# Kernel optimization log

Measured on AMD Instinct MI355X. Metric: run time of the kernel, lower is better.

The kernel has to match this reference:

```python
import jax, jax.numpy as jnp
import numpy as np

B, L, C = 2, 2048, 1024
H = 16
HD = C // H  # head_features = 64


def setup_inputs() -> dict:
    key = jax.random.key(0)
    k1, k2, k3, k4, k5, k6 = jax.random.split(key, 6)
    input_x = jax.random.normal(k1, (B, L, C), dtype=jnp.float32)
    x_mask = jax.random.randint(k2, (B, 1, 1, L), 0, 2, dtype=jnp.int32)
    s = 1.0 / np.sqrt(C)
    W_qkv = jax.random.normal(k3, (C, 3 * C), dtype=jnp.float32) * s
    b_qkv = jax.random.normal(k4, (3 * C,), dtype=jnp.float32) * 0.01
    W_proj = jax.random.normal(k5, (C, C), dtype=jnp.float32) * s
    b_proj = jax.random.normal(k6, (C,), dtype=jnp.float32) * 0.01
    return {"input_x": input_x, "x_mask": x_mask, "W_qkv": W_qkv,
            "b_qkv": b_qkv, "W_proj": W_proj, "b_proj": b_proj}


def reference(input_x, x_mask, W_qkv, b_qkv, W_proj, b_proj):
    # qkv projection: [B,L,3C] -> [3,B,H,L,HD]
    qkv = input_x @ W_qkv + b_qkv
    qkv = qkv.reshape(B, L, 3, H, HD).transpose(2, 0, 3, 1, 4)
    q, k, v = qkv[0], qkv[1], qkv[2]
    q = q * (HD ** -0.5)  # first scale (module applies it to q)
    scores = jnp.einsum('bhld,bhmd->bhlm', q, k)  # [B,H,L,L]
    scores = jnp.where(x_mask == 1, jnp.float32(-1e10), scores)
    scores = scores / jnp.sqrt(jnp.float32(HD))  # module's second scale (faithful quirk)
    probs = jax.nn.softmax(scores, axis=-1)
    out = jnp.einsum('bhlm,bhmd->bhld', probs, v)  # [B,H,L,HD]
    out = out.transpose(0, 2, 1, 3).reshape(B, L, C)
    return out @ W_proj + b_proj
```

## Files before the change

kernel.cpp:

```cpp
#include <hip/hip_runtime.h>
#include <stdint.h>

typedef __attribute__((ext_vector_type(8))) short short8;
typedef __attribute__((ext_vector_type(4))) short short4v;
typedef __attribute__((ext_vector_type(4))) float floatx4;
typedef __attribute__((ext_vector_type(16))) float floatx16;

#define B_ 2
#define L_ 2048
#define C_ 1024
#define H_ 16
#define HD_ 64

#define QSCALE (0.015625f * 1.44269504088896f)
#define MASKVAL (-1.8033688e9f)

__device__ __forceinline__ unsigned short f2bf(float f) {
  union { float f; uint32_t u; } v; v.f = f;
  uint32_t r = 0x7FFFu + ((v.u >> 16) & 1u);
  return (unsigned short)((v.u + r) >> 16);
}

__device__ __forceinline__ uint32_t cvtpk(float lo, float hi) {
  uint32_t r;
  asm("v_cvt_pk_bf16_f32 %0, %1, %2" : "=v"(r) : "v"(lo), "v"(hi));
  return r;
}

__device__ __forceinline__ unsigned short f2bf_hw(float f) {
  return (unsigned short)cvtpk(f, f);
}

__device__ __forceinline__ void pl32swap(uint32_t& a, uint32_t& b) {
  asm volatile("v_permlane32_swap_b32 %0, %1" : "+v"(a), "+v"(b));
}

__device__ __forceinline__ void async16(const void* g, void* l) {
  __builtin_amdgcn_global_load_lds(
      (const __attribute__((address_space(1))) void*)g,
      (__attribute__((address_space(3))) void*)l, 16, 0, 0);
}

__global__ __launch_bounds__(256) void cast_bf16_k(const float* __restrict__ in,
                                                   unsigned short* __restrict__ out, int n) {
  int i = (blockIdx.x * 256 + threadIdx.x) * 8;
  if (i >= n) return;
  floatx4 a = *(const floatx4*)(in + i);
  floatx4 b = *(const floatx4*)(in + i + 4);
  short8 o;
  o[0] = (short)f2bf(a[0]); o[1] = (short)f2bf(a[1]);
  o[2] = (short)f2bf(a[2]); o[3] = (short)f2bf(a[3]);
  o[4] = (short)f2bf(b[0]); o[5] = (short)f2bf(b[1]);
  o[6] = (short)f2bf(b[2]); o[7] = (short)f2bf(b[3]);
  *(short8*)(out + i) = o;
}

__global__ __launch_bounds__(256) void transpose_cast_k(const float* __restrict__ in,
                                                        unsigned short* __restrict__ out,
                                                        int R, int Cc) {
  __shared__ float tile[32][33];
  int tx = threadIdx.x, ty = threadIdx.y;
  int c0 = blockIdx.x * 32, r0 = blockIdx.y * 32;
#pragma unroll
  for (int i = 0; i < 4; i++)
    tile[ty + i * 8][tx] = in[(r0 + ty + i * 8) * Cc + c0 + tx];
  __syncthreads();
#pragma unroll
  for (int i = 0; i < 4; i++)
    out[(c0 + ty + i * 8) * R + r0 + tx] = f2bf(tile[tx][ty + i * 8]);
}

__global__ __launch_bounds__(256) void maskpre_k(const int* __restrict__ mask,
                                                 unsigned short* __restrict__ maskbf) {
  int i = blockIdx.x * 256 + threadIdx.x;
  if (i < B_ * L_) maskbf[i] = (mask[i] == 1) ? f2bf(MASKVAL) : (unsigned short)0;
}

template <int EPI, int BN>
__global__ __launch_bounds__(256) void gemm128(const unsigned short* __restrict__ A,
                                               const unsigned short* __restrict__ BT, int K,
                                               int nbx,
                                               const float* __restrict__ bias,
                                               unsigned short* __restrict__ outQ,
                                               unsigned short* __restrict__ outK,
                                               unsigned short* __restrict__ outVT,
                                               float* __restrict__ outF) {
  __shared__ __attribute__((aligned(16))) unsigned short Asmem[2][128 * 32];
  __shared__ __attribute__((aligned(16))) unsigned short Bsmem[2][BN * 32];
  const int t = threadIdx.x;
  const int wave = t >> 6, lane = t & 63;
  const int wr = wave >> 1, wc = wave & 1;
  const int NW = BN / 2;
  const int NF = BN / 32;
  const int nwg = gridDim.x;
  const int id = (blockIdx.x & 7) * (nwg >> 3) + (blockIdx.x >> 3);
  const int bx = id % nbx, by = id / nbx;
  const int row0 = by * 128, col0 = bx * BN;

  const int arow = row0 + (t >> 2), brow = col0 + (t >> 2);
  const int koff = (t & 3) * 8;

#define STAGE(buf, k0)                                                                 \
  {                                                                                    \
    async16(A + (size_t)arow * K + (k0) + koff, &Asmem[buf][t * 8]);                   \
    async16(A + (size_t)(arow + 64) * K + (k0) + koff, &Asmem[buf][(256 + t) * 8]);    \
    async16(BT + (size_t)brow * K + (k0) + koff, &Bsmem[buf][t * 8]);                  \
    if (BN == 128)                                                                     \
      async16(BT + (size_t)(brow + 64) * K + (k0) + koff, &Bsmem[buf][(256 + t) * 8]); \
  }

  floatx4 acc[4][NF] = {};
  STAGE(0, 0);
  __syncthreads();
  int cur = 0;
  for (int k0 = 0; k0 < K; k0 += 32) {
    if (k0 + 32 < K) STAGE(cur ^ 1, k0 + 32);
    short8 af[4], bfr[NF];
#pragma unroll
    for (int m = 0; m < 4; m++)
      af[m] = *(const short8*)(&Asmem[cur][(wr * 64 + m * 16 + (lane & 15)) * 32 +
                                           (lane >> 4) * 8]);
#pragma unroll
    for (int n = 0; n < NF; n++)
      bfr[n] = *(const short8*)(&Bsmem[cur][(wc * NW + n * 16 + (lane & 15)) * 32 +
                                            (lane >> 4) * 8]);
#pragma unroll
    for (int m = 0; m < 4; m++)
#pragma unroll
      for (int n = 0; n < NF; n++)
        acc[m][n] = __builtin_amdgcn_mfma_f32_16x16x32_bf16(af[m], bfr[n], acc[m][n], 0, 0, 0);
    __syncthreads();
    cur ^= 1;
  }
#undef STAGE

#pragma unroll
  for (int m = 0; m < 4; m++)
#pragma unroll
    for (int n = 0; n < NF; n++) {
      const int r0e = row0 + wr * 64 + m * 16 + (lane >> 4) * 4;
      const int cc = col0 + wc * NW + n * 16 + (lane & 15);
      const float bv = bias[cc];
      if (EPI == 2) {
#pragma unroll
        for (int j = 0; j < 4; j++)
          outF[(size_t)(r0e + j) * C_ + cc] = acc[m][n][j] + bv;
      } else {
        const int which = col0 >> 10;
        const int rem = cc & 1023, h = rem >> 6, d = rem & 63;
        const int bb = r0e >> 11, l0 = r0e & 2047;
        const size_t base = (size_t)(bb * H_ + h) * (L_ * HD_);
        if (which == 0) {
#pragma unroll
          for (int j = 0; j < 4; j++)
            outQ[base + (size_t)(l0 + j) * HD_ + d] = f2bf_hw((acc[m][n][j] + bv) * QSCALE);
        } else if (which == 1) {
          const size_t kbase =
              base + ((l0 >> 5) * 8 + (d >> 4) * 2 + ((d >> 3) & 1)) * 256 + (d & 7);
#pragma unroll
          for (int j = 0; j < 4; j++)
            outK[kbase + ((l0 & 31) + j) * 8] = f2bf_hw(acc[m][n][j] + bv);
        } else {
          const size_t vbase = base +
                               ((((l0 >> 7) * 2 + (d >> 5)) * 8 + ((l0 >> 4) & 7)) * 2 +
                                ((l0 >> 3) & 1)) * 256 +
                               (d & 31) * 8 + (l0 & 7);
          union { unsigned short s[4]; short4v v; } ov;
#pragma unroll
          for (int j = 0; j < 4; j++) ov.s[j] = f2bf_hw(acc[m][n][j] + bv);
          *(short4v*)(outVT + vbase) = ov.v;
        }
      }
    }
}

__global__ __launch_bounds__(256) void attn_k(const unsigned short* __restrict__ Q,
                                              const unsigned short* __restrict__ Kf,
                                              const unsigned short* __restrict__ VTf,
                                              const unsigned short* __restrict__ maskbf,
                                              unsigned short* __restrict__ attn_out) {
  __shared__ __attribute__((aligned(16))) unsigned short Ks[128 * 64];
  __shared__ __attribute__((aligned(16))) unsigned short VTs[64 * 128];
  __shared__ __attribute__((aligned(16))) unsigned short maskLb[L_];

  const int t = threadIdx.x, wave = t >> 6, lane = t & 63;
  const int h = lane >> 5, c32 = lane & 31;
  const int bh = blockIdx.x & 31;
  const int qt = blockIdx.x >> 5;
  const int b = bh >> 4, hh = bh & 15;
  const unsigned short* Qp = Q + (size_t)bh * L_ * HD_;
  const unsigned short* Kp = Kf + (size_t)bh * L_ * HD_;
  const unsigned short* VTp = VTf + (size_t)bh * L_ * HD_;
  const int qrow = qt * 128 + wave * 32 + c32;

  short8 qf[4];
#pragma unroll
  for (int ks = 0; ks < 4; ks++)
    qf[ks] = *(const short8*)(Qp + (size_t)qrow * HD_ + ks * 16 + h * 8);

  union { uint32_t u[4]; short8 v; } onef;
  onef.u[0] = h ? 0u : 0x3F80u;
  onef.u[1] = 0; onef.u[2] = 0; onef.u[3] = 0;
  floatx16 z16;
#pragma unroll
  for (int e = 0; e < 16; e++) z16[e] = 0.f;

  async16(maskbf + b * L_ + t * 8, maskLb + t * 8);

  floatx16 o[2] = {};
  float lrun = 0.f;

  for (int kv = 0; kv < 16; kv++) {
    __syncthreads();
#pragma unroll
    for (int i = 0; i < 4; i++) {
      int idx = i * 256 + t;
      async16(Kp + (size_t)kv * 8192 + idx * 8, Ks + idx * 8);
    }
#pragma unroll
    for (int i = 0; i < 4; i++) {
      int idx = i * 256 + t;
      async16(VTp + (size_t)kv * 8192 + idx * 8, VTs + idx * 8);
    }
    __syncthreads();

    floatx16 s[4];
#pragma unroll
    for (int kg = 0; kg < 4; kg++) {
      union { uint32_t u[4]; short8 v; } mf;
      unsigned short mval = maskLb[kv * 128 + kg * 32 + c32];
      mf.u[0] = h ? 0u : (uint32_t)mval;
      mf.u[1] = 0; mf.u[2] = 0; mf.u[3] = 0;
      s[kg] = __builtin_amdgcn_mfma_f32_32x32x16_bf16(mf.v, onef.v, z16, 0, 0, 0);
#pragma unroll
      for (int ks = 0; ks < 4; ks++) {
        const short8 kfr = *(const short8*)(Ks + ((kg * 4 + ks) * 2 + h) * 256 + c32 * 8);
        s[kg] = __builtin_amdgcn_mfma_f32_32x32x16_bf16(kfr, qf[ks], s[kg], 0, 0, 0);
      }
    }

    float r0 = 0.f, r1 = 0.f, r2 = 0.f, r3 = 0.f;
#pragma unroll
    for (int kg = 0; kg < 4; kg++)
#pragma unroll
      for (int q = 0; q < 4; q++) {
        float p0 = __builtin_amdgcn_exp2f(s[kg][4 * q + 0]);
        float p1 = __builtin_amdgcn_exp2f(s[kg][4 * q + 1]);
        float p2 = __builtin_amdgcn_exp2f(s[kg][4 * q + 2]);
        float p3 = __builtin_amdgcn_exp2f(s[kg][4 * q + 3]);
        s[kg][4 * q + 0] = p0; s[kg][4 * q + 1] = p1;
        s[kg][4 * q + 2] = p2; s[kg][4 * q + 3] = p3;
        r0 += p0; r1 += p1; r2 += p2; r3 += p3;
      }
    float rs = (r0 + r1) + (r2 + r3);
    rs += __shfl_xor(rs, 32);
    lrun += rs;

#pragma unroll
    for (int kg = 0; kg < 4; kg++) {
      uint32_t pk[8];
#pragma unroll
      for (int e = 0; e < 8; e++) pk[e] = cvtpk(s[kg][2 * e], s[kg][2 * e + 1]);
#pragma unroll
      for (int ts = 0; ts < 2; ts++) {
        uint32_t x0 = pk[4 * ts + 0], x1 = pk[4 * ts + 1];
        uint32_t y0 = pk[4 * ts + 2], y1 = pk[4 * ts + 3];
        pl32swap(x0, y0);
        pl32swap(x1, y1);
        union { uint32_t u[4]; short8 v; } pf;
        pf.u[0] = x0; pf.u[1] = x1; pf.u[2] = y0; pf.u[3] = y1;
        const int kt = kg * 2 + ts;
#pragma unroll
        for (int dg = 0; dg < 2; dg++) {
          const short8 vfr =
              *(const short8*)(VTs + ((dg * 8 + kt) * 2 + h) * 256 + c32 * 8);
          o[dg] = __builtin_amdgcn_mfma_f32_32x32x16_bf16(vfr, pf.v, o[dg], 0, 0, 0);
        }
      }
    }
  }

  const float inv = 1.f / lrun;
#pragma unroll
  for (int dg = 0; dg < 2; dg++)
#pragma unroll
    for (int rr = 0; rr < 4; rr++) {
      short4v ov;
#pragma unroll
      for (int jj = 0; jj < 4; jj++) ov[jj] = (short)f2bf(o[dg][rr * 4 + jj] * inv);
      int d0 = dg * 32 + rr * 8 + h * 4;
      *(short4v*)(attn_out + ((size_t)b * L_ + qrow) * C_ + hh * HD_ + d0) = ov;
    }
}

extern "C" void kernel_launch(void* const* d_in, const int* in_sizes, int n_in,
                              void* d_out, int out_size, void* d_ws, size_t ws_size,
                              hipStream_t stream) {
  const float* x = (const float*)d_in[0];
  const int* mask = (const int*)d_in[1];
  const float* Wqkv = (const float*)d_in[2];
  const float* bqkv = (const float*)d_in[3];
  const float* Wproj = (const float*)d_in[4];
  const float* bproj = (const float*)d_in[5];
  float* out = (float*)d_out;
  char* ws = (char*)d_ws;

  unsigned short* Xb = (unsigned short*)(ws);
  unsigned short* WqkvT = (unsigned short*)(ws + (8u << 20));
  unsigned short* WprojT = (unsigned short*)(ws + (14u << 20));
  unsigned short* Qb = (unsigned short*)(ws + (16u << 20));
  unsigned short* Kb = (unsigned short*)(ws + (24u << 20));
  unsigned short* VTb = (unsigned short*)(ws + (32u << 20));
  unsigned short* AOb = Xb;
  unsigned short* maskbf = (unsigned short*)(ws + (8u << 20));

  cast_bf16_k<<<(B_ * L_ * C_) / 8 / 256, 256, 0, stream>>>(x, Xb, B_ * L_ * C_);
  dim3 tb(32, 8);
  transpose_cast_k<<<dim3(3 * C_ / 32, C_ / 32), tb, 0, stream>>>(Wqkv, WqkvT, C_, 3 * C_);
  transpose_cast_k<<<dim3(C_ / 32, C_ / 32), tb, 0, stream>>>(Wproj, WprojT, C_, C_);

  gemm128<1, 128><<<768, 256, 0, stream>>>(Xb, WqkvT, C_, 24, bqkv, Qb, Kb, VTb, nullptr);

  maskpre_k<<<(B_ * L_) / 256, 256, 0, stream>>>(mask, maskbf);

  attn_k<<<B_ * H_ * (L_ / 128), 256, 0, stream>>>(Qb, Kb, VTb, maskbf, AOb);

  gemm128<2, 64><<<512, 256, 0, stream>>>(AOb, WprojT, C_, 16, bproj, nullptr, nullptr, nullptr,
                                          out);
}
```

Baseline: 118.1 us.

## Fuse prep kernels and load two KV tiles per attention barrier

New measurement: 116.7 us. Within noise of the previous version (-1.1%).

```diff
diff --git a/kernel.cpp b/kernel.cpp
--- a/kernel.cpp
+++ b/kernel.cpp
@@ -41,39 +41,52 @@
       (__attribute__((address_space(3))) void*)l, 16, 0, 0);
 }
 
-__global__ __launch_bounds__(256) void cast_bf16_k(const float* __restrict__ in,
-                                                   unsigned short* __restrict__ out, int n) {
-  int i = (blockIdx.x * 256 + threadIdx.x) * 8;
-  if (i >= n) return;
-  floatx4 a = *(const floatx4*)(in + i);
-  floatx4 b = *(const floatx4*)(in + i + 4);
-  short8 o;
-  o[0] = (short)f2bf(a[0]); o[1] = (short)f2bf(a[1]);
-  o[2] = (short)f2bf(a[2]); o[3] = (short)f2bf(a[3]);
-  o[4] = (short)f2bf(b[0]); o[5] = (short)f2bf(b[1]);
-  o[6] = (short)f2bf(b[2]); o[7] = (short)f2bf(b[3]);
-  *(short8*)(out + i) = o;
-}
-
-__global__ __launch_bounds__(256) void transpose_cast_k(const float* __restrict__ in,
-                                                        unsigned short* __restrict__ out,
-                                                        int R, int Cc) {
-  __shared__ float tile[32][33];
-  int tx = threadIdx.x, ty = threadIdx.y;
-  int c0 = blockIdx.x * 32, r0 = blockIdx.y * 32;
-#pragma unroll
-  for (int i = 0; i < 4; i++)
-    tile[ty + i * 8][tx] = in[(r0 + ty + i * 8) * Cc + c0 + tx];
-  __syncthreads();
-#pragma unroll
-  for (int i = 0; i < 4; i++)
-    out[(c0 + ty + i * 8) * R + r0 + tx] = f2bf(tile[tx][ty + i * 8]);
+__global__ __launch_bounds__(256) void prep_k(const float* __restrict__ x,
+                                              unsigned short* __restrict__ Xb,
+                                              const int* __restrict__ mask,
+                                              unsigned short* __restrict__ maskbf) {
+  int bid = blockIdx.x;
+  if (bid < 2048) {
+    int i = (bid * 256 + threadIdx.x) * 8;
+    floatx4 a = *(const floatx4*)(x + i);
+    floatx4 b = *(const floatx4*)(x + i + 4);
+    short8 o;
+    o[0] = (short)f2bf(a[0]); o[1] = (short)f2bf(a[1]);
+    o[2] = (short)f2bf(a[2]); o[3] = (short)f2bf(a[3]);
+    o[4] = (short)f2bf(b[0]); o[5] = (short)f2bf(b[1]);
+    o[6] = (short)f2bf(b[2]); o[7] = (short)f2bf(b[3]);
+    *(short8*)(Xb + i) = o;
+  } else if (maskbf) {
+    int i = (bid - 2048) * 256 + threadIdx.x;
+    if (i < B_ * L_) maskbf[i] = (mask[i] == 1) ? f2bf(MASKVAL) : (unsigned short)0;
+  }
 }
 
 __global__ __launch_bounds__(256) void maskpre_k(const int* __restrict__ mask,
                                                  unsigned short* __restrict__ maskbf) {
   int i = blockIdx.x * 256 + threadIdx.x;
   if (i < B_ * L_) maskbf[i] = (mask[i] == 1) ? f2bf(MASKVAL) : (unsigned short)0;
+}
+
+__global__ __launch_bounds__(256) void transpose2_k(const float* __restrict__ W1,
+                                                    unsigned short* __restrict__ O1,
+                                                    const float* __restrict__ W2,
+                                                    unsigned short* __restrict__ O2) {
+  const int z = blockIdx.z;
+  if (z == 1 && blockIdx.x >= C_ / 32) return;
+  const float* in = z ? W2 : W1;
+  unsigned short* out = z ? O2 : O1;
+  const int Cc = z ? C_ : 3 * C_;
+  __shared__ float tile[32][33];
+  int tx = threadIdx.x, ty = threadIdx.y;
+  int c0 = blockIdx.x * 32, r0 = blockIdx.y * 32;
+#pragma unroll
+  for (int i = 0; i < 4; i++)
+    tile[ty + i * 8][tx] = in[(r0 + ty + i * 8) * Cc + c0 + tx];
+  __syncthreads();
+#pragma unroll
+  for (int i = 0; i < 4; i++)
+    out[(c0 + ty + i * 8) * C_ + r0 + tx] = f2bf(tile[tx][ty + i * 8]);
 }
 
 template <int EPI, int BN>
@@ -179,8 +192,8 @@
                                               const unsigned short* __restrict__ VTf,
                                               const unsigned short* __restrict__ maskbf,
                                               unsigned short* __restrict__ attn_out) {
-  __shared__ __attribute__((aligned(16))) unsigned short Ks[128 * 64];
-  __shared__ __attribute__((aligned(16))) unsigned short VTs[64 * 128];
+  __shared__ __attribute__((aligned(16))) unsigned short Ks[2 * 128 * 64];
+  __shared__ __attribute__((aligned(16))) unsigned short VTs[2 * 64 * 128];
   __shared__ __attribute__((aligned(16))) unsigned short maskLb[L_];
 
   const int t = threadIdx.x, wave = t >> 6, lane = t & 63;
@@ -210,75 +223,74 @@
   floatx16 o[2] = {};
   float lrun = 0.f;
 
-  for (int kv = 0; kv < 16; kv++) {
+#define COMPUTE(KSB, VTB, MOFF)                                                        \
+  {                                                                                    \
+    floatx16 s[4];                                                                     \
+    _Pragma("unroll") for (int kg = 0; kg < 4; kg++) {                                 \
+      union { uint32_t u[4]; short8 v; } mf;                                           \
+      unsigned short mval = maskLb[(MOFF) + kg * 32 + c32];                            \
+      mf.u[0] = h ? 0u : (uint32_t)mval;                                               \
+      mf.u[1] = 0; mf.u[2] = 0; mf.u[3] = 0;                                           \
+      s[kg] = __builtin_amdgcn_mfma_f32_32x32x16_bf16(mf.v, onef.v, z16, 0, 0, 0);     \
+      _Pragma("unroll") for (int ks = 0; ks < 4; ks++) {                               \
+        const short8 kfr =                                                             \
+            *(const short8*)((KSB) + ((kg * 4 + ks) * 2 + h) * 256 + c32 * 8);         \
+        s[kg] = __builtin_amdgcn_mfma_f32_32x32x16_bf16(kfr, qf[ks], s[kg], 0, 0, 0);  \
+      }                                                                                \
+    }                                                                                  \
+    float r0 = 0.f, r1 = 0.f, r2 = 0.f, r3 = 0.f;                                      \
+    _Pragma("unroll") for (int kg = 0; kg < 4; kg++)                                   \
+        _Pragma("unroll") for (int q = 0; q < 4; q++) {                                \
+      float p0 = __builtin_amdgcn_exp2f(s[kg][4 * q + 0]);                             \
+      float p1 = __builtin_amdgcn_exp2f(s[kg][4 * q + 1]);                             \
+      float p2 = __builtin_amdgcn_exp2f(s[kg][4 * q + 2]);                             \
+      float p3 = __builtin_amdgcn_exp2f(s[kg][4 * q + 3]);                             \
+      s[kg][4 * q + 0] = p0; s[kg][4 * q + 1] = p1;                                    \
+      s[kg][4 * q + 2] = p2; s[kg][4 * q + 3] = p3;                                    \
+      r0 += p0; r1 += p1; r2 += p2; r3 += p3;                                          \
+    }                                                                                  \
+    float rs = (r0 + r1) + (r2 + r3);                                                  \
+    rs += __shfl_xor(rs, 32);                                                          \
+    lrun += rs;                                                                        \
+    _Pragma("unroll") for (int kg = 0; kg < 4; kg++) {                                 \
+      uint32_t pk[8];                                                                  \
+      _Pragma("unroll") for (int e = 0; e < 8; e++)                                    \
+          pk[e] = cvtpk(s[kg][2 * e], s[kg][2 * e + 1]);                               \
+      _Pragma("unroll") for (int ts = 0; ts < 2; ts++) {                               \
+        uint32_t x0 = pk[4 * ts + 0], x1 = pk[4 * ts + 1];                             \
+        uint32_t y0 = pk[4 * ts + 2], y1 = pk[4 * ts + 3];                             \
+        pl32swap(x0, y0);                                                              \
+        pl32swap(x1, y1);                                                              \
+        union { uint32_t u[4]; short8 v; } pf;                                         \
+        pf.u[0] = x0; pf.u[1] = x1; pf.u[2] = y0; pf.u[3] = y1;                        \
+        const int kt = kg * 2 + ts;                                                    \
+        _Pragma("unroll") for (int dg = 0; dg < 2; dg++) {                             \
+          const short8 vfr =                                                           \
+              *(const short8*)((VTB) + ((dg * 8 + kt) * 2 + h) * 256 + c32 * 8);       \
+          o[dg] = __builtin_amdgcn_mfma_f32_32x32x16_bf16(vfr, pf.v, o[dg], 0, 0, 0);  \
+        }                                                                              \
+      }                                                                                \
+    }                                                                                  \
+  }
+
+  for (int kvp = 0; kvp < 8; kvp++) {
     __syncthreads();
 #pragma unroll
-    for (int i = 0; i < 4; i++) {
+    for (int i = 0; i < 8; i++) {
       int idx = i * 256 + t;
-      async16(Kp + (size_t)kv * 8192 + idx * 8, Ks + idx * 8);
+      async16(Kp + (size_t)kvp * 16384 + idx * 8, Ks + idx * 8);
     }
 #pragma unroll
-    for (int i = 0; i < 4; i++) {
+    for (int i = 0; i < 8; i++) {
       int idx = i * 256 + t;
-      async16(VTp + (size_t)kv * 8192 + idx * 8, VTs + idx * 8);
+      async16(VTp + (size_t)kvp * 16384 + idx * 8, VTs + idx * 8);
     }
     __syncthreads();
 
-    floatx16 s[4];
-#pragma unroll
-    for (int kg = 0; kg < 4; kg++) {
-      union { uint32_t u[4]; short8 v; } mf;
-      unsigned short mval = maskLb[kv * 128 + kg * 32 + c32];
-      mf.u[0] = h ? 0u : (uint32_t)mval;
-      mf.u[1] = 0; mf.u[2] = 0; mf.u[3] = 0;
-      s[kg] = __builtin_amdgcn_mfma_f32_32x32x16_bf16(mf.v, onef.v, z16, 0, 0, 0);
-#pragma unroll
-      for (int ks = 0; ks < 4; ks++) {
-        const short8 kfr = *(const short8*)(Ks + ((kg * 4 + ks) * 2 + h) * 256 + c32 * 8);
-        s[kg] = __builtin_amdgcn_mfma_f32_32x32x16_bf16(kfr, qf[ks], s[kg], 0, 0, 0);
-      }
-    }
-
-    float r0 = 0.f, r1 = 0.f, r2 = 0.f, r3 = 0.f;
-#pragma unroll
-    for (int kg = 0; kg < 4; kg++)
-#pragma unroll
-      for (int q = 0; q < 4; q++) {
-        float p0 = __builtin_amdgcn_exp2f(s[kg][4 * q + 0]);
-        float p1 = __builtin_amdgcn_exp2f(s[kg][4 * q + 1]);
-        float p2 = __builtin_amdgcn_exp2f(s[kg][4 * q + 2]);
-        float p3 = __builtin_amdgcn_exp2f(s[kg][4 * q + 3]);
-        s[kg][4 * q + 0] = p0; s[kg][4 * q + 1] = p1;
-        s[kg][4 * q + 2] = p2; s[kg][4 * q + 3] = p3;
-        r0 += p0; r1 += p1; r2 += p2; r3 += p3;
-      }
-    float rs = (r0 + r1) + (r2 + r3);
-    rs += __shfl_xor(rs, 32);
-    lrun += rs;
-
-#pragma unroll
-    for (int kg = 0; kg < 4; kg++) {
-      uint32_t pk[8];
-#pragma unroll
-      for (int e = 0; e < 8; e++) pk[e] = cvtpk(s[kg][2 * e], s[kg][2 * e + 1]);
-#pragma unroll
-      for (int ts = 0; ts < 2; ts++) {
-        uint32_t x0 = pk[4 * ts + 0], x1 = pk[4 * ts + 1];
-        uint32_t y0 = pk[4 * ts + 2], y1 = pk[4 * ts + 3];
-        pl32swap(x0, y0);
-        pl32swap(x1, y1);
-        union { uint32_t u[4]; short8 v; } pf;
-        pf.u[0] = x0; pf.u[1] = x1; pf.u[2] = y0; pf.u[3] = y1;
-        const int kt = kg * 2 + ts;
-#pragma unroll
-        for (int dg = 0; dg < 2; dg++) {
-          const short8 vfr =
-              *(const short8*)(VTs + ((dg * 8 + kt) * 2 + h) * 256 + c32 * 8);
-          o[dg] = __builtin_amdgcn_mfma_f32_32x32x16_bf16(vfr, pf.v, o[dg], 0, 0, 0);
-        }
-      }
-    }
-  }
+    COMPUTE(Ks, VTs, kvp * 256);
+    COMPUTE(Ks + 8192, VTs + 8192, kvp * 256 + 128);
+  }
+#undef COMPUTE
 
   const float inv = 1.f / lrun;
 #pragma unroll
@@ -312,16 +324,19 @@
   unsigned short* Kb = (unsigned short*)(ws + (24u << 20));
   unsigned short* VTb = (unsigned short*)(ws + (32u << 20));
   unsigned short* AOb = Xb;
-  unsigned short* maskbf = (unsigned short*)(ws + (8u << 20));
-
-  cast_bf16_k<<<(B_ * L_ * C_) / 8 / 256, 256, 0, stream>>>(x, Xb, B_ * L_ * C_);
+
+  const bool fused_mask = ws_size >= ((size_t)(40u << 20) + 8192);
+  unsigned short* maskbf = fused_mask ? (unsigned short*)(ws + (40u << 20))
+                                      : (unsigned short*)(ws + (8u << 20));
+
+  prep_k<<<2064, 256, 0, stream>>>(x, Xb, mask, fused_mask ? maskbf : nullptr);
+
   dim3 tb(32, 8);
-  transpose_cast_k<<<dim3(3 * C_ / 32, C_ / 32), tb, 0, stream>>>(Wqkv, WqkvT, C_, 3 * C_);
-  transpose_cast_k<<<dim3(C_ / 32, C_ / 32), tb, 0, stream>>>(Wproj, WprojT, C_, C_);
+  transpose2_k<<<dim3(3 * C_ / 32, C_ / 32, 2), tb, 0, stream>>>(Wqkv, WqkvT, Wproj, WprojT);
 
   gemm128<1, 128><<<768, 256, 0, stream>>>(Xb, WqkvT, C_, 24, bqkv, Qb, Kb, VTb, nullptr);
 
-  maskpre_k<<<(B_ * L_) / 256, 256, 0, stream>>>(mask, maskbf);
+  if (!fused_mask) maskpre_k<<<(B_ * L_) / 256, 256, 0, stream>>>(mask, maskbf);
 
   attn_k<<<B_ * H_ * (L_ / 128), 256, 0, stream>>>(Qb, Kb, VTb, maskbf, AOb);
 
```
